# Optimization experiments

Hardware: AMD Instinct MI355X
Metric: run time of the kernel (lower is better)

Reference implementation:

```python
import jax, jax.numpy as jnp
import numpy as np

D_MODEL = 1024
N_HEADS = 16
D_K = D_MODEL // N_HEADS


def setup_inputs() -> dict:
    key = jax.random.key(0)
    ks = jax.random.split(key, 7)
    B, T = 4, 2048
    scale = 1.0 / np.sqrt(D_MODEL)
    x = jax.random.normal(ks[0], (B, T, D_MODEL), dtype=jnp.float32)
    Wq = jax.random.uniform(ks[1], (D_MODEL, D_MODEL), jnp.float32, -scale, scale)
    Wk = jax.random.uniform(ks[2], (D_MODEL, D_MODEL), jnp.float32, -scale, scale)
    Wv = jax.random.uniform(ks[3], (D_MODEL, D_MODEL), jnp.float32, -scale, scale)
    bq = jax.random.uniform(ks[4], (D_MODEL,), jnp.float32, -scale, scale)
    bk = jax.random.uniform(ks[5], (D_MODEL,), jnp.float32, -scale, scale)
    bv = jax.random.uniform(ks[6], (D_MODEL,), jnp.float32, -scale, scale)
    return {"x": x, "Wq": Wq, "bq": bq, "Wk": Wk, "bk": bk, "Wv": Wv, "bv": bv}


def reference(x, Wq, bq, Wk, bk, Wv, bv):
    B, T, _ = x.shape
    # QKV projections -> (B, H, T, d_k)
    def split_heads(y):
        return y.reshape(B, T, N_HEADS, D_K).transpose(0, 2, 1, 3)
    Q = split_heads(x @ Wq + bq)
    K = split_heads(x @ Wk + bk)
    V = split_heads(x @ Wv + bv)
    scores = jnp.einsum('bhqd,bhkd->bhqk', Q, K) / jnp.sqrt(jnp.float32(D_K))
    # additive causal mask: -inf above the diagonal
    causal = jnp.tril(jnp.ones((T, T), dtype=bool))
    scores = jnp.where(causal, scores, -jnp.inf)
    attn = jax.nn.softmax(scores, axis=-1)
    out = jnp.einsum('bhqk,bhkd->bhqd', attn, V)
    return out.transpose(0, 2, 1, 3).reshape(B, T, D_MODEL)
```

## Files before the change

kernel.cpp:

```cpp
#include <hip/hip_runtime.h>
#include <hip/hip_bf16.h>

#define DM 1024
#define NH 16
#define DK 64
#define TT 2048
#define NBATCH 4
#define BT 8192

typedef __attribute__((ext_vector_type(8))) short short8;
typedef __attribute__((ext_vector_type(4))) float f32x4;
typedef unsigned short u16;

#define MFMA(a,b,c) __builtin_amdgcn_mfma_f32_16x16x32_bf16((a),(b),(c),0,0,0)

#define QSCALE 0.18033688011112684f

#define EXP2(x) __builtin_amdgcn_exp2f(x)

__device__ __forceinline__ u16 f2bf(float f){
  union { float f; unsigned u; } v; v.f = f;
  return (u16)((v.u + 0x7fffu + ((v.u >> 16) & 1u)) >> 16);
}

__device__ __forceinline__ unsigned cvtpk(float lo, float hi){
  unsigned r;
  asm("v_cvt_pk_bf16_f32 %0, %1, %2" : "=v"(r) : "v"(lo), "v"(hi));
  return r;
}

__device__ __forceinline__ void gload16(const void* g, void* l){
  __builtin_amdgcn_global_load_lds((__attribute__((address_space(1))) void*)(g),
                                   (__attribute__((address_space(3))) void*)(l), 16, 0, 0);
}

__device__ __forceinline__ float plmax(float x){
#if __has_builtin(__builtin_amdgcn_permlane16_swap) && __has_builtin(__builtin_amdgcn_permlane32_swap)
  auto r = __builtin_amdgcn_permlane16_swap(__float_as_uint(x), __float_as_uint(x), false, false);
  x = fmaxf(__uint_as_float(r[0]), __uint_as_float(r[1]));
  auto r2 = __builtin_amdgcn_permlane32_swap(__float_as_uint(x), __float_as_uint(x), false, false);
  x = fmaxf(__uint_as_float(r2[0]), __uint_as_float(r2[1]));
#else
  x = fmaxf(x, __shfl_xor(x, 16, 64));
  x = fmaxf(x, __shfl_xor(x, 32, 64));
#endif
  return x;
}

__device__ __forceinline__ float plsum(float x){
#if __has_builtin(__builtin_amdgcn_permlane16_swap) && __has_builtin(__builtin_amdgcn_permlane32_swap)
  auto r = __builtin_amdgcn_permlane16_swap(__float_as_uint(x), __float_as_uint(x), false, false);
  x = __uint_as_float(r[0]) + __uint_as_float(r[1]);
  auto r2 = __builtin_amdgcn_permlane32_swap(__float_as_uint(x), __float_as_uint(x), false, false);
  x = __uint_as_float(r2[0]) + __uint_as_float(r2[1]);
#else
  x = x + __shfl_xor(x, 16, 64);
  x = x + __shfl_xor(x, 32, 64);
#endif
  return x;
}

__global__ __launch_bounds__(256) void cvt_x(const float* __restrict__ x, u16* __restrict__ xb){
  int i = (blockIdx.x * 256 + threadIdx.x) * 4;
  float4 v = *(const float4*)(x + i);
  u16 o0 = f2bf(v.x), o1 = f2bf(v.y), o2 = f2bf(v.z), o3 = f2bf(v.w);
  ushort4 o; o.x=o0; o.y=o1; o.z=o2; o.w=o3;
  *(ushort4*)(xb + i) = o;
}

__global__ __launch_bounds__(256) void twp(
    const float* __restrict__ Wq, const float* __restrict__ Wk, const float* __restrict__ Wv,
    u16* __restrict__ wtq, u16* __restrict__ wtk, u16* __restrict__ wtv){
  const float* W = (blockIdx.z == 0) ? Wq : (blockIdx.z == 1) ? Wk : Wv;
  u16* wt = (blockIdx.z == 0) ? wtq : (blockIdx.z == 1) ? wtk : wtv;
  __shared__ float tile[32][33];
  int k0 = blockIdx.x * 32, n0 = blockIdx.y * 32;
  int tx = threadIdx.x & 31, ty = threadIdx.x >> 5;
  #pragma unroll
  for(int r = ty; r < 32; r += 8)
    tile[r][tx] = W[(size_t)(k0 + r) * DM + n0 + tx];
  __syncthreads();
  #pragma unroll
  for(int r = ty; r < 32; r += 8)
    wt[(size_t)(n0 + r) * DM + k0 + tx] = f2bf(tile[tx][r]);
}

__global__ __launch_bounds__(256) void qkv_gemm(
    const u16* __restrict__ xb,
    const u16* __restrict__ wtq, const u16* __restrict__ wtk, const u16* __restrict__ wtv,
    const float* __restrict__ bq, const float* __restrict__ bk, const float* __restrict__ bv,
    u16* __restrict__ qws, u16* __restrict__ kws, u16* __restrict__ vtws){
  __shared__ u16 sa[128 * 64];
  __shared__ u16 sb[128 * 64];
  const int id = blockIdx.x;
  const int idx = id >> 3;
  const int mt = (id & 7) * 8 + (idx & 7);
  const int y  = idx >> 3;
  const int m0 = mt * 128;
  const int ng = y * 128;
  const int mat = ng >> 10;
  const int n0 = ng & 1023;
  const u16* wt = (mat == 0) ? wtq : (mat == 1) ? wtk : wtv;
  const float* bias = (mat == 0) ? bq : (mat == 1) ? bk : bv;
  const int tid = threadIdx.x;
  const int lane = tid & 63, w = tid >> 6;
  const int wm = (w >> 1) * 64, wn = (w & 1) * 64;
  const int wbase0 = tid & 192;

  f32x4 acc[4][4] = {};

  for(int k0 = 0; k0 < 1024; k0 += 64){
    #pragma unroll
    for(int p = 0; p < 4; p++){
      int base = p * 256 + wbase0;
      int idx2 = base + lane;
      int row = idx2 >> 3;
      int chs = (idx2 & 7) ^ (row & 7);
      gload16(xb + (size_t)(m0 + row) * 1024 + k0 + chs * 8, (char*)sa + base * 16);
      gload16(wt + (size_t)(n0 + row) * 1024 + k0 + chs * 8, (char*)sb + base * 16);
    }
    __syncthreads();
    #pragma unroll
    for(int ks = 0; ks < 2; ks++){
      short8 af[4], bfr[4];
      #pragma unroll
      for(int i = 0; i < 4; i++){
        int ra = wm + i * 16 + (lane & 15);
        int ca = ks * 64 + (lane >> 4) * 16;
        af[i] = *(const short8*)((const char*)sa + ra * 128 + (ca ^ ((ra & 7) << 4)));
        int rb = wn + i * 16 + (lane & 15);
        bfr[i] = *(const short8*)((const char*)sb + rb * 128 + (ca ^ ((rb & 7) << 4)));
      }
      __builtin_amdgcn_s_setprio(1);
      #pragma unroll
      for(int i = 0; i < 4; i++)
        #pragma unroll
        for(int j = 0; j < 4; j++)
          acc[i][j] = MFMA(af[i], bfr[j], acc[i][j]);
      __builtin_amdgcn_s_setprio(0);
    }
    __syncthreads();
  }

  const float scl = (mat == 0) ? QSCALE : 1.0f;
  #pragma unroll
  for(int j = 0; j < 4; j++){
    int n = n0 + wn + j * 16 + (lane & 15);
    float bv_ = bias[n];
    int h = n >> 6, d = n & 63;
    #pragma unroll
    for(int i = 0; i < 4; i++){
      int mb = m0 + wm + i * 16 + (lane >> 4) * 4;
      int b = mb >> 11, t = mb & 2047;
      int bh = b * NH + h;
      if(mat == 2){
        ushort4 o4;
        o4.x = f2bf(acc[i][j][0] + bv_);
        o4.y = f2bf(acc[i][j][1] + bv_);
        o4.z = f2bf(acc[i][j][2] + bv_);
        o4.w = f2bf(acc[i][j][3] + bv_);
        int tp = (t & ~31) | (((t >> 2) & 3) << 3) | (((t >> 4) & 1) << 2);
        *(ushort4*)(vtws + ((size_t)bh * DK + d) * TT + tp) = o4;
      } else {
        u16* dst = (mat == 0) ? qws : kws;
        #pragma unroll
        for(int r = 0; r < 4; r++){
          u16 o = f2bf((acc[i][j][r] + bv_) * scl);
          dst[((size_t)bh * TT + t + r) * DK + d] = o;
        }
      }
    }
  }
}

__global__ __launch_bounds__(512) void attn(
    const u16* __restrict__ qws, const u16* __restrict__ kws, const u16* __restrict__ vtws,
    float* __restrict__ out){
  __shared__ u16 kt[2][64 * 64];
  __shared__ u16 vt[2][64 * 64];

  const int id = blockIdx.x;
  const int swz = (id & 7) * 64 + (id >> 3);
  const int qx = swz & 7;
  const int bh = swz >> 3;

  const int tid = threadIdx.x, lane = tid & 63, w = tid >> 6;
  const int g = lane >> 4, ln = lane & 15;
  const int b = bh >> 4, h = bh & 15;
  const u16* kbase = kws + (size_t)bh * TT * DK;
  const u16* vbase = vtws + (size_t)bh * DK * TT;
  const int sbase = tid & 448;
  const int srow = tid >> 3;
  const int schs = (tid & 7) ^ (srow & 7);

  #pragma unroll 1
  for(int qi = 0; qi < 2; qi++){
    const int qt = qi ? (15 - qx) : qx;
    const int q = qt * 128 + w * 16 + ln;

    short8 qf[2];
    {
      const u16* gq = qws + ((size_t)bh * TT + q) * DK + g * 8;
      qf[0] = *(const short8*)gq;
      qf[1] = *(const short8*)(gq + 32);
    }

    f32x4 o[4] = {};
    float m = -INFINITY, l = 0.f;

    const int nkt = 2 * qt + 2;
    const int myNkt = nkt - (w < 4 ? 1 : 0);

    __syncthreads();
    gload16(kbase + (size_t)srow * DK + schs * 8, (char*)kt[0] + sbase * 16);
    gload16(vbase + (size_t)srow * TT + schs * 8, (char*)vt[0] + sbase * 16);

    #pragma unroll 1
    for(int kti = 0; kti < nkt; kti++){
      const int cur = kti & 1;
      __syncthreads();

      if(kti + 1 < nkt){
        const int k0n = (kti + 1) * 64;
        gload16(kbase + (size_t)(k0n + srow) * DK + schs * 8, (char*)kt[cur ^ 1] + sbase * 16);
        gload16(vbase + (size_t)srow * TT + k0n + schs * 8, (char*)vt[cur ^ 1] + sbase * 16);
      }

      if(kti < myNkt){
        f32x4 s[4];
        __builtin_amdgcn_s_setprio(1);
        #pragma unroll
        for(int i = 0; i < 4; i++){
          f32x4 c = {};
          #pragma unroll
          for(int ks = 0; ks < 2; ks++){
            int rb = i * 16 + ln;
            int cb = ks * 64 + g * 16;
            short8 kfr = *(const short8*)((const char*)kt[cur] + rb * 128 + (cb ^ ((rb & 7) << 4)));
            c = MFMA(kfr, qf[ks], c);
          }
          s[i] = c;
        }
        __builtin_amdgcn_s_setprio(0);

        if(kti == myNkt - 1){
          const int k0 = kti * 64;
          #pragma unroll
          for(int i = 0; i < 4; i++)
            #pragma unroll
            for(int r = 0; r < 4; r++)
              if(k0 + i * 16 + g * 4 + r > q) s[i][r] = -INFINITY;
        }

        float mx0 = fmaxf(fmaxf(s[0][0], s[0][1]), fmaxf(s[0][2], s[0][3]));
        float mx1 = fmaxf(fmaxf(s[1][0], s[1][1]), fmaxf(s[1][2], s[1][3]));
        float mx2 = fmaxf(fmaxf(s[2][0], s[2][1]), fmaxf(s[2][2], s[2][3]));
        float mx3 = fmaxf(fmaxf(s[3][0], s[3][1]), fmaxf(s[3][2], s[3][3]));
        float pmax = fmaxf(fmaxf(mx0, mx1), fmaxf(mx2, mx3));
        pmax = plmax(pmax);

        if(!__all(pmax <= m + 8.f)){
          float mnew = fmaxf(m, pmax);
          float alpha = EXP2(m - mnew);
          l *= alpha;
          #pragma unroll
          for(int i = 0; i < 4; i++)
            #pragma unroll
            for(int r = 0; r < 4; r++) o[i][r] *= alpha;
          m = mnew;
        }

        #pragma unroll
        for(int i = 0; i < 4; i++)
          #pragma unroll
          for(int r = 0; r < 4; r++){
            float p = EXP2(s[i][r] - m);
            s[i][r] = p; l += p;
          }

        union PU { short8 s8; unsigned w[4]; };
        PU pb[2];
        #pragma unroll
        for(int ks = 0; ks < 2; ks++){
          pb[ks].w[0] = cvtpk(s[2*ks][0],   s[2*ks][1]);
          pb[ks].w[1] = cvtpk(s[2*ks][2],   s[2*ks][3]);
          pb[ks].w[2] = cvtpk(s[2*ks+1][0], s[2*ks+1][1]);
          pb[ks].w[3] = cvtpk(s[2*ks+1][2], s[2*ks+1][3]);
        }

        __builtin_amdgcn_s_setprio(1);
        #pragma unroll
        for(int i = 0; i < 4; i++){
          int dr = i * 16 + ln;
          const char* vrow = (const char*)vt[cur] + dr * 128;
          int sw = (dr & 7) << 4;
          #pragma unroll
          for(int ks = 0; ks < 2; ks++){
            short8 av = *(const short8*)(vrow + ((64 * ks + g * 16) ^ sw));
            o[i] = MFMA(av, pb[ks].s8, o[i]);
          }
        }
        __builtin_amdgcn_s_setprio(0);
      }
    }

    l = plsum(l);
    float inv = 1.0f / l;
    float* orow = out + ((size_t)(b * TT + q)) * DM + h * 64 + g * 4;
    #pragma unroll
    for(int i = 0; i < 4; i++){
      float4 v4;
      v4.x = o[i][0] * inv; v4.y = o[i][1] * inv;
      v4.z = o[i][2] * inv; v4.w = o[i][3] * inv;
      *(float4*)(orow + i * 16) = v4;
    }
  }
}

extern "C" void kernel_launch(void* const* d_in, const int* in_sizes, int n_in,
                              void* d_out, int out_size, void* d_ws, size_t ws_size,
                              hipStream_t stream){
  const float* x  = (const float*)d_in[0];
  const float* Wq = (const float*)d_in[1];
  const float* bq = (const float*)d_in[2];
  const float* Wk = (const float*)d_in[3];
  const float* bk = (const float*)d_in[4];
  const float* Wv = (const float*)d_in[5];
  const float* bv = (const float*)d_in[6];
  float* out = (float*)d_out;

  char* ws = (char*)d_ws;
  u16* xb   = (u16*)(ws);
  u16* wtq  = (u16*)(ws + (16u << 20));
  u16* wtk  = (u16*)(ws + (18u << 20));
  u16* wtv  = (u16*)(ws + (20u << 20));
  u16* qws  = (u16*)(ws + (22u << 20));
  u16* kws  = (u16*)(ws + (38u << 20));
  u16* vtws = (u16*)(ws + (54u << 20));

  cvt_x<<<dim3(BT * DM / 1024), dim3(256), 0, stream>>>(x, xb);
  twp<<<dim3(32, 32, 3), dim3(256), 0, stream>>>(Wq, Wk, Wv, wtq, wtk, wtv);
  qkv_gemm<<<dim3(1536), dim3(256), 0, stream>>>(xb, wtq, wtk, wtv, bq, bk, bv, qws, kws, vtws);
  attn<<<dim3(512), dim3(512), 0, stream>>>(qws, kws, vtws, out);
}
```

Measured before the change: 147.7 us.

## Replace QKV GEMM with 256x256-tile double-buffered 8-wave pipelined kernel

Replaces the 128x128 single-buffered QKV projection GEMM with a 256x256 tile kernel using 8 waves and 128KB of dynamic LDS double-buffering. The next K-slice is prefetched while MFMAs run on the current buffer, and each K step is split into four phases with fragment reuse and explicit barriers. Larger tiles cut global traffic per FLOP and the prefetch hides load latency. In exchange it runs one block per CU, 384 blocks on the grid, and uses more registers for the accumulators.

```diff
diff --git a/kernel.cpp b/kernel.cpp
--- a/kernel.cpp
+++ b/kernel.cpp
@@ -85,72 +85,111 @@
     wt[(size_t)(n0 + r) * DM + k0 + tx] = f2bf(tile[tx][r]);
 }
 
-__global__ __launch_bounds__(256) void qkv_gemm(
+#define STAGE(TT_, LB_) { \
+  int kk_ = (TT_) * 64; \
+  _Pragma("unroll") \
+  for(int p_ = 0; p_ < 4; p_++){ \
+    int base_ = p_ * 512 + (tid & 448); \
+    int ci_ = base_ + lane; \
+    int row_ = ci_ >> 3, chs_ = (ci_ & 7) ^ (row_ & 7); \
+    gload16(xb + (size_t)(m0 + row_) * 1024 + kk_ + chs_ * 8, (LB_) + base_ * 16); \
+  } \
+  _Pragma("unroll") \
+  for(int p_ = 0; p_ < 4; p_++){ \
+    int base_ = p_ * 512 + (tid & 448); \
+    int ci_ = base_ + lane; \
+    int row_ = ci_ >> 3, chs_ = (ci_ & 7) ^ (row_ & 7); \
+    gload16(wt + (size_t)(n0 + row_) * 1024 + kk_ + chs_ * 8, (LB_) + 32768 + base_ * 16); \
+  } }
+
+#define PHASE(LB_, RH, CH, RA, RB) { \
+  const char* A_ = (LB_); const char* B_ = (LB_) + 32768; \
+  if(RA){ \
+    _Pragma("unroll") \
+    for(int i2 = 0; i2 < 4; i2++){ \
+      int ra_ = wm + ((RH)*4 + i2) * 16 + ln; int swa_ = (ra_ & 7) << 4; \
+      af[i2][0] = *(const short8*)(A_ + ra_ * 128 + ((g * 16) ^ swa_)); \
+      af[i2][1] = *(const short8*)(A_ + ra_ * 128 + ((64 + g * 16) ^ swa_)); \
+    } } \
+  if(RB){ \
+    _Pragma("unroll") \
+    for(int j2 = 0; j2 < 2; j2++){ \
+      int rb_ = wn + ((CH)*2 + j2) * 16 + ln; int swb_ = (rb_ & 7) << 4; \
+      bf[j2][0] = *(const short8*)(B_ + rb_ * 128 + ((g * 16) ^ swb_)); \
+      bf[j2][1] = *(const short8*)(B_ + rb_ * 128 + ((64 + g * 16) ^ swb_)); \
+    } } \
+  __builtin_amdgcn_s_barrier(); \
+  asm volatile("s_waitcnt lgkmcnt(0)" ::: "memory"); \
+  __builtin_amdgcn_sched_barrier(0); \
+  __builtin_amdgcn_s_setprio(1); \
+  _Pragma("unroll") \
+  for(int ks2 = 0; ks2 < 2; ks2++) \
+    _Pragma("unroll") \
+    for(int i2 = 0; i2 < 4; i2++) \
+      _Pragma("unroll") \
+      for(int j2 = 0; j2 < 2; j2++) \
+        acc[(RH)*4+i2][(CH)*2+j2] = MFMA(af[i2][ks2], bf[j2][ks2], acc[(RH)*4+i2][(CH)*2+j2]); \
+  __builtin_amdgcn_s_setprio(0); \
+  __builtin_amdgcn_s_barrier(); }
+
+__global__ __launch_bounds__(512, 1) void qkv8(
     const u16* __restrict__ xb,
     const u16* __restrict__ wtq, const u16* __restrict__ wtk, const u16* __restrict__ wtv,
     const float* __restrict__ bq, const float* __restrict__ bk, const float* __restrict__ bv,
     u16* __restrict__ qws, u16* __restrict__ kws, u16* __restrict__ vtws){
-  __shared__ u16 sa[128 * 64];
-  __shared__ u16 sb[128 * 64];
+  extern __shared__ char smem[];
+  char* b0 = smem;
+  char* b1 = smem + 65536;
+
   const int id = blockIdx.x;
-  const int idx = id >> 3;
-  const int mt = (id & 7) * 8 + (idx & 7);
-  const int y  = idx >> 3;
-  const int m0 = mt * 128;
-  const int ng = y * 128;
-  const int mat = ng >> 10;
-  const int n0 = ng & 1023;
+  const int xcd = id & 7, local = id >> 3;
+  const int mt = xcd * 4 + (local & 3);
+  const int panel = local >> 2;
+  const int m0 = mt * 256;
+  const int mat = panel >> 2;
+  const int n0 = (panel & 3) * 256;
   const u16* wt = (mat == 0) ? wtq : (mat == 1) ? wtk : wtv;
   const float* bias = (mat == 0) ? bq : (mat == 1) ? bk : bv;
-  const int tid = threadIdx.x;
-  const int lane = tid & 63, w = tid >> 6;
-  const int wm = (w >> 1) * 64, wn = (w & 1) * 64;
-  const int wbase0 = tid & 192;
-
-  f32x4 acc[4][4] = {};
-
-  for(int k0 = 0; k0 < 1024; k0 += 64){
-    #pragma unroll
-    for(int p = 0; p < 4; p++){
-      int base = p * 256 + wbase0;
-      int idx2 = base + lane;
-      int row = idx2 >> 3;
-      int chs = (idx2 & 7) ^ (row & 7);
-      gload16(xb + (size_t)(m0 + row) * 1024 + k0 + chs * 8, (char*)sa + base * 16);
-      gload16(wt + (size_t)(n0 + row) * 1024 + k0 + chs * 8, (char*)sb + base * 16);
-    }
-    __syncthreads();
-    #pragma unroll
-    for(int ks = 0; ks < 2; ks++){
-      short8 af[4], bfr[4];
-      #pragma unroll
-      for(int i = 0; i < 4; i++){
-        int ra = wm + i * 16 + (lane & 15);
-        int ca = ks * 64 + (lane >> 4) * 16;
-        af[i] = *(const short8*)((const char*)sa + ra * 128 + (ca ^ ((ra & 7) << 4)));
-        int rb = wn + i * 16 + (lane & 15);
-        bfr[i] = *(const short8*)((const char*)sb + rb * 128 + (ca ^ ((rb & 7) << 4)));
-      }
-      __builtin_amdgcn_s_setprio(1);
-      #pragma unroll
-      for(int i = 0; i < 4; i++)
-        #pragma unroll
-        for(int j = 0; j < 4; j++)
-          acc[i][j] = MFMA(af[i], bfr[j], acc[i][j]);
-      __builtin_amdgcn_s_setprio(0);
-    }
-    __syncthreads();
+
+  const int tid = threadIdx.x, lane = tid & 63, w = tid >> 6;
+  const int g = lane >> 4, ln = lane & 15;
+  const int wm = (w >> 2) * 128;
+  const int wn = (w & 3) * 64;
+
+  f32x4 acc[8][4] = {};
+  short8 af[4][2], bf[2][2];
+
+  STAGE(0, b0);
+
+  #pragma unroll 1
+  for(int it = 0; it < 8; it++){
+    const int t = 2 * it;
+    STAGE((t + 1) & 15, b1);
+    asm volatile("s_waitcnt vmcnt(8)" ::: "memory");
+    __builtin_amdgcn_s_barrier();
+    PHASE(b0, 0, 0, 1, 1)
+    PHASE(b0, 1, 0, 1, 0)
+    PHASE(b0, 1, 1, 0, 1)
+    PHASE(b0, 0, 1, 1, 0)
+    STAGE((t + 2) & 15, b0);
+    asm volatile("s_waitcnt vmcnt(8)" ::: "memory");
+    __builtin_amdgcn_s_barrier();
+    PHASE(b1, 0, 0, 1, 1)
+    PHASE(b1, 1, 0, 1, 0)
+    PHASE(b1, 1, 1, 0, 1)
+    PHASE(b1, 0, 1, 1, 0)
   }
+  asm volatile("s_waitcnt vmcnt(0)" ::: "memory");
 
   const float scl = (mat == 0) ? QSCALE : 1.0f;
   #pragma unroll
   for(int j = 0; j < 4; j++){
-    int n = n0 + wn + j * 16 + (lane & 15);
+    int n = n0 + wn + j * 16 + ln;
     float bv_ = bias[n];
     int h = n >> 6, d = n & 63;
     #pragma unroll
-    for(int i = 0; i < 4; i++){
-      int mb = m0 + wm + i * 16 + (lane >> 4) * 4;
+    for(int i = 0; i < 8; i++){
+      int mb = m0 + wm + i * 16 + g * 4;
       int b = mb >> 11, t = mb & 2047;
       int bh = b * NH + h;
       if(mat == 2){
@@ -338,8 +377,15 @@
   u16* kws  = (u16*)(ws + (38u << 20));
   u16* vtws = (u16*)(ws + (54u << 20));
 
+  static bool qkv8_init = false;
+  if(!qkv8_init){
+    hipFuncSetAttribute((const void*)qkv8,
+                        hipFuncAttributeMaxDynamicSharedMemorySize, 131072);
+    qkv8_init = true;
+  }
+
   cvt_x<<<dim3(BT * DM / 1024), dim3(256), 0, stream>>>(x, xb);
   twp<<<dim3(32, 32, 3), dim3(256), 0, stream>>>(Wq, Wk, Wv, wtq, wtk, wtv);
-  qkv_gemm<<<dim3(1536), dim3(256), 0, stream>>>(xb, wtq, wtk, wtv, bq, bk, bv, qws, kws, vtws);
+  qkv8<<<dim3(384), dim3(512), 131072, stream>>>(xb, wtq, wtk, wtv, bq, bk, bv, qws, kws, vtws);
   attn<<<dim3(512), dim3(512), 0, stream>>>(qws, kws, vtws, out);
 }
```

Result: slower. 155.7 us (+5.5%).
